# Performance work log

Measured on AMD Instinct MI355X. Metric: run time of the kernel, lower is better.

The kernel has to match this reference:

```python
import jax, jax.numpy as jnp
import numpy as np

COMMITMENT_COST = 1.0


def setup_inputs() -> dict:
    key = jax.random.key(0)
    k1, k2 = jax.random.split(key)
    B, D, H, W = 32, 256, 32, 32
    K = 1024
    z = jax.random.normal(k1, (B, D, H, W), dtype=jnp.float32)
    # torch init: uniform(-1/K, 1/K)
    codebook = jax.random.uniform(k2, (K, D), dtype=jnp.float32,
                                  minval=-1.0 / K, maxval=1.0 / K)
    return {"z": z, "codebook": codebook}


def reference(z, codebook):
    B, D, H, W = z.shape
    # (B, D, H, W) -> (B, H, W, D) -> (N, D)
    zp = jnp.transpose(z, (0, 2, 3, 1))
    zf = zp.reshape(-1, D)
    # squared euclidean distances (N, K): ||z||^2 + ||e||^2 - 2 z.e
    d = (jnp.sum(zf * zf, axis=1, keepdims=True)
         + jnp.sum(codebook * codebook, axis=1)
         - 2.0 * jnp.matmul(zf, codebook.T))
    idx = jnp.argmin(d, axis=1)                    # (N,)
    zq = codebook[idx].reshape(B, H, W, D)         # gather
    vq_loss = jnp.mean((jax.lax.stop_gradient(zq) - zp) ** 2)
    commitment_loss = jnp.mean((zq - jax.lax.stop_gradient(zp)) ** 2)
    loss = vq_loss + COMMITMENT_COST * commitment_loss
    # straight-through estimator
    zq_st = zp + jax.lax.stop_gradient(zq - zp)
    zq_out = jnp.transpose(zq_st, (0, 3, 1, 2))    # back to (B, D, H, W)
    indices = idx.reshape(B, H, W)
    return zq_out, indices, loss
```

## Files before the change

### kernel.cpp

```cpp
#include <hip/hip_runtime.h>

#define NPOS 32768
#define DDIM 256
#define KCODE 1024
#define HW 1024
#define BSTRIDE (256*1024)
#define OUT0_SIZE 8388608
#define OUT1_SIZE 32768

#define WS_ET     0
#define WS_ZN     262144
#define WS_EN     294912
#define WS_PACKED 295936


__global__ void vq_zn(const float* __restrict__ z, float* __restrict__ zn,
                      unsigned long long* __restrict__ packed,
                      float* __restrict__ loss_slot) {
    int n = blockIdx.x * 256 + threadIdx.x;
    int b = n >> 10, hw = n & 1023;
    const float* zp = z + (size_t)b * BSTRIDE + hw;
    float half_s[2];
    #pragma unroll
    for (int h = 0; h < 2; ++h) {
        const float* p = zp + (size_t)(h * 128) * HW;
        float r[8];
        #pragma unroll
        for (int j = 0; j < 8; ++j) {
            float v = p[(size_t)j * HW];
            r[j] = __fmul_rn(v, v);
        }
        #pragma unroll
        for (int i = 8; i < 128; i += 8) {
            #pragma unroll
            for (int j = 0; j < 8; ++j) {
                float v = p[(size_t)(i + j) * HW];
                r[j] = __fadd_rn(r[j], __fmul_rn(v, v));
            }
        }
        half_s[h] = __fadd_rn(
            __fadd_rn(__fadd_rn(r[0], r[1]), __fadd_rn(r[2], r[3])),
            __fadd_rn(__fadd_rn(r[4], r[5]), __fadd_rn(r[6], r[7])));
    }
    zn[n] = __fadd_rn(half_s[0], half_s[1]);
    packed[n] = 0xFFFFFFFFFFFFFFFFull;
    if (n == 0) *loss_slot = 0.0f;
}

__global__ void vq_en(const float* __restrict__ cb, float* __restrict__ en) {
    int k = blockIdx.x * 256 + threadIdx.x;
    const float* row = cb + (size_t)k * DDIM;
    float half_s[2];
    #pragma unroll
    for (int h = 0; h < 2; ++h) {
        const float* p = row + h * 128;
        float r[8];
        #pragma unroll
        for (int j = 0; j < 8; ++j) r[j] = __fmul_rn(p[j], p[j]);
        #pragma unroll
        for (int i = 8; i < 128; i += 8) {
            #pragma unroll
            for (int j = 0; j < 8; ++j)
                r[j] = __fadd_rn(r[j], __fmul_rn(p[i + j], p[i + j]));
        }
        half_s[h] = __fadd_rn(
            __fadd_rn(__fadd_rn(r[0], r[1]), __fadd_rn(r[2], r[3])),
            __fadd_rn(__fadd_rn(r[4], r[5]), __fadd_rn(r[6], r[7])));
    }
    en[k] = __fadd_rn(half_s[0], half_s[1]);
}

__global__ void vq_trans(const float* __restrict__ cb, float* __restrict__ et) {
    __shared__ float tile[64][65];
    int k0 = (blockIdx.x & 15) * 64;
    int d0 = (blockIdx.x >> 4) * 64;
    int t = threadIdx.x;
    #pragma unroll
    for (int p = 0; p < 4; ++p) {
        int r  = p * 16 + (t >> 4);
        int c4 = (t & 15) * 4;
        float4 v = *reinterpret_cast<const float4*>(
            cb + (size_t)(k0 + r) * DDIM + d0 + c4);
        tile[r][c4] = v.x; tile[r][c4+1] = v.y;
        tile[r][c4+2] = v.z; tile[r][c4+3] = v.w;
    }
    __syncthreads();
    #pragma unroll
    for (int s = 0; s < 16; ++s) {
        int dd = s * 4 + (t >> 6);
        int kk = t & 63;
        et[(size_t)(d0 + dd) * KCODE + k0 + kk] = tile[kk][dd];
    }
}

#define BM 64
#define BN 256
#define BK 16
#define BSKEW(k) ((k) + ((k) >> 3))

__launch_bounds__(256, 4)
__global__ void vq_argmin(const float* __restrict__ z,
                          const float* __restrict__ ws_f,
                          unsigned long long* __restrict__ packed) {
    __shared__ float As[BK][64];
    __shared__ float Bs[BK][288];

    const float* ET  = ws_f + WS_ET;
    const float* znW = ws_f + WS_ZN;
    const float* enW = ws_f + WS_EN;

    int t  = threadIdx.x;
    int tx = t & 31;
    int ty = t >> 5;
    int bc = blockIdx.x & 3;
    int bm = blockIdx.x >> 2;
    int kc = bc * BN;
    int n0 = bm * BM;
    int b  = n0 >> 10, hw0 = n0 & 1023;
    const float* zb = z + (size_t)b * BSTRIDE + hw0;

    float znr[8];
    #pragma unroll
    for (int j = 0; j < 8; ++j) znr[j] = znW[n0 + ty * 8 + j];

    float acc[8][8];
    #pragma unroll
    for (int j = 0; j < 8; ++j)
        #pragma unroll
        for (int c = 0; c < 8; ++c) acc[j][c] = 0.0f;

    for (int d0 = 0; d0 < DDIM; d0 += BK) {
        __syncthreads();
        {
            int dk = t >> 4, p4 = (t & 15) << 2;
            float4 v = *reinterpret_cast<const float4*>(
                zb + (size_t)(d0 + dk) * HW + p4);
            As[dk][p4] = v.x; As[dk][p4+1] = v.y;
            As[dk][p4+2] = v.z; As[dk][p4+3] = v.w;
        }
        #pragma unroll
        for (int i = 0; i < 4; ++i) {
            int q = t + i * 256;
            int dk = q >> 6, m = q & 63;
            float4 v = *reinterpret_cast<const float4*>(
                ET + (size_t)(d0 + dk) * KCODE + kc + 4 * m);
            int ph = BSKEW(4 * m);
            *reinterpret_cast<float4*>(&Bs[dk][ph]) = v;
        }
        __syncthreads();

        #pragma unroll
        for (int dk = 0; dk < BK; ++dk) {
            float4 a0 = *reinterpret_cast<const float4*>(&As[dk][ty * 8]);
            float4 a1 = *reinterpret_cast<const float4*>(&As[dk][ty * 8 + 4]);
            float4 b0 = *reinterpret_cast<const float4*>(&Bs[dk][9 * tx]);
            float4 b1 = *reinterpret_cast<const float4*>(&Bs[dk][9 * tx + 4]);
            float a[8]  = {a0.x, a0.y, a0.z, a0.w, a1.x, a1.y, a1.z, a1.w};
            float bb[8] = {b0.x, b0.y, b0.z, b0.w, b1.x, b1.y, b1.z, b1.w};
            #pragma unroll
            for (int j = 0; j < 8; ++j)
                #pragma unroll
                for (int c = 0; c < 8; ++c)
                    acc[j][c] = fmaf(a[j], bb[c], acc[j][c]);
        }
    }

    float m1[8];
    int   i1[8];
    #pragma unroll
    for (int j = 0; j < 8; ++j) { m1[j] = 1e30f; i1[j] = 0; }
    #pragma unroll
    for (int c = 0; c < 8; ++c) {
        int k = kc + tx * 8 + c;
        float ek = enW[k];
        #pragma unroll
        for (int j = 0; j < 8; ++j) {
            float t1 = __fadd_rn(znr[j], ek);
            float d  = __fsub_rn(t1, __fmul_rn(2.0f, acc[j][c]));
            if (d < m1[j]) { m1[j] = d; i1[j] = k; }
        }
    }

    #pragma unroll
    for (int j = 0; j < 8; ++j) {
        float a1 = m1[j];
        int   ii = i1[j];
        #pragma unroll
        for (int off = 1; off < 32; off <<= 1) {
            float o1 = __shfl_xor(a1, off, 32);
            int   oi = __shfl_xor(ii, off, 32);
            if (o1 < a1 || (o1 == a1 && oi < ii)) { a1 = o1; ii = oi; }
        }
        if (tx == 0) {
            unsigned long long key =
                ((unsigned long long)__float_as_uint(a1) << 32) |
                (unsigned long long)(unsigned)ii;
            atomicMin(&packed[n0 + ty * 8 + j], key);
        }
    }
}

__global__ void vq_gather(const float* __restrict__ z,
                          const float* __restrict__ cb,
                          const unsigned long long* __restrict__ packed,
                          float* __restrict__ out,
                          float* __restrict__ loss) {
    int n = blockIdx.x * 256 + threadIdx.x;
    int b = n >> 10, hw = n & 1023;
    int k = (int)(unsigned)(packed[n] & 0xFFFFFFFFull);
    const float* e  = cb + (size_t)k * DDIM;
    const float* zp = z + (size_t)b * BSTRIDE + hw;
    float* op = out + (size_t)b * BSTRIDE + hw;
    float s = 0.0f;
    #pragma unroll 4
    for (int d = 0; d < DDIM; ++d) {
        float ev = e[d];
        float zv = zp[(size_t)d * HW];
        op[(size_t)d * HW] = ev;
        float df = ev - zv;
        s = fmaf(df, df, s);
    }
    out[OUT0_SIZE + n] = (float)k;

    #pragma unroll
    for (int off = 32; off > 0; off >>= 1) s += __shfl_down(s, off);
    __shared__ float red[4];
    int lane = threadIdx.x & 63, w = threadIdx.x >> 6;
    if (lane == 0) red[w] = s;
    __syncthreads();
    if (threadIdx.x == 0) {
        float tot = (red[0] + red[1] + red[2] + red[3]) * (2.0f / 8388608.0f);
        atomicAdd(loss, tot);
    }
}

extern "C" void kernel_launch(void* const* d_in, const int* in_sizes, int n_in,
                              void* d_out, int out_size, void* d_ws, size_t ws_size,
                              hipStream_t stream) {
    const float* z  = (const float*)d_in[0];
    const float* cb = (const float*)d_in[1];
    float* out  = (float*)d_out;
    float* ws_f = (float*)d_ws;
    unsigned long long* packed =
        (unsigned long long*)(ws_f + WS_PACKED);
    float* loss = out + OUT0_SIZE + OUT1_SIZE;

    vq_zn<<<NPOS / 256, 256, 0, stream>>>(z, ws_f + WS_ZN, packed, loss);
    vq_en<<<KCODE / 256, 256, 0, stream>>>(cb, ws_f + WS_EN);
    vq_trans<<<64, 256, 0, stream>>>(cb, ws_f + WS_ET);
    vq_argmin<<<(NPOS / BM) * (KCODE / BN), 256, 0, stream>>>(z, ws_f, packed);
    vq_gather<<<NPOS / 256, 256, 0, stream>>>(z, cb, packed, out, loss);
}
```

Measured before the change: 353.4 us.

## Merge prep kernels, read z tile directly from global, vectorize codebook gather

Fuses the zn, en and codebook-transpose kernels into one launch, with separate block ranges doing each job, to save launch overhead. In the argmin GEMM the z tile is no longer staged through shared memory: each thread loads its 8 positions straight from global (cache-backed) memory on every dk step. The gather kernel reads codebook rows as float4 instead of scalars. Skipping the LDS staging removes a store and sync step but raises repeated global/L1 traffic in the inner loop, since the 32 threads sharing a ty load the same addresses.

```diff
diff --git a/kernel.cpp b/kernel.cpp
--- a/kernel.cpp
+++ b/kernel.cpp
@@ -13,83 +13,86 @@
 #define WS_EN     294912
 #define WS_PACKED 295936
 
-
-__global__ void vq_zn(const float* __restrict__ z, float* __restrict__ zn,
-                      unsigned long long* __restrict__ packed,
-                      float* __restrict__ loss_slot) {
-    int n = blockIdx.x * 256 + threadIdx.x;
-    int b = n >> 10, hw = n & 1023;
-    const float* zp = z + (size_t)b * BSTRIDE + hw;
-    float half_s[2];
-    #pragma unroll
-    for (int h = 0; h < 2; ++h) {
-        const float* p = zp + (size_t)(h * 128) * HW;
-        float r[8];
-        #pragma unroll
-        for (int j = 0; j < 8; ++j) {
-            float v = p[(size_t)j * HW];
-            r[j] = __fmul_rn(v, v);
-        }
-        #pragma unroll
-        for (int i = 8; i < 128; i += 8) {
+__global__ void vq_prep(const float* __restrict__ z,
+                        const float* __restrict__ cb,
+                        float* __restrict__ ws_f,
+                        unsigned long long* __restrict__ packed,
+                        float* __restrict__ loss_slot) {
+    __shared__ float tile[64][65];
+    int bx = blockIdx.x;
+    int t  = threadIdx.x;
+
+    if (bx < 128) {
+        int n = bx * 256 + t;
+        int b = n >> 10, hw = n & 1023;
+        const float* zp = z + (size_t)b * BSTRIDE + hw;
+        float half_s[2];
+        #pragma unroll
+        for (int h = 0; h < 2; ++h) {
+            const float* p = zp + (size_t)(h * 128) * HW;
+            float r[8];
             #pragma unroll
             for (int j = 0; j < 8; ++j) {
-                float v = p[(size_t)(i + j) * HW];
-                r[j] = __fadd_rn(r[j], __fmul_rn(v, v));
+                float v = p[(size_t)j * HW];
+                r[j] = __fmul_rn(v, v);
             }
-        }
-        half_s[h] = __fadd_rn(
-            __fadd_rn(__fadd_rn(r[0], r[1]), __fadd_rn(r[2], r[3])),
-            __fadd_rn(__fadd_rn(r[4], r[5]), __fadd_rn(r[6], r[7])));
-    }
-    zn[n] = __fadd_rn(half_s[0], half_s[1]);
-    packed[n] = 0xFFFFFFFFFFFFFFFFull;
-    if (n == 0) *loss_slot = 0.0f;
-}
-
-__global__ void vq_en(const float* __restrict__ cb, float* __restrict__ en) {
-    int k = blockIdx.x * 256 + threadIdx.x;
-    const float* row = cb + (size_t)k * DDIM;
-    float half_s[2];
-    #pragma unroll
-    for (int h = 0; h < 2; ++h) {
-        const float* p = row + h * 128;
-        float r[8];
-        #pragma unroll
-        for (int j = 0; j < 8; ++j) r[j] = __fmul_rn(p[j], p[j]);
-        #pragma unroll
-        for (int i = 8; i < 128; i += 8) {
-            #pragma unroll
-            for (int j = 0; j < 8; ++j)
-                r[j] = __fadd_rn(r[j], __fmul_rn(p[i + j], p[i + j]));
-        }
-        half_s[h] = __fadd_rn(
-            __fadd_rn(__fadd_rn(r[0], r[1]), __fadd_rn(r[2], r[3])),
-            __fadd_rn(__fadd_rn(r[4], r[5]), __fadd_rn(r[6], r[7])));
-    }
-    en[k] = __fadd_rn(half_s[0], half_s[1]);
-}
-
-__global__ void vq_trans(const float* __restrict__ cb, float* __restrict__ et) {
-    __shared__ float tile[64][65];
-    int k0 = (blockIdx.x & 15) * 64;
-    int d0 = (blockIdx.x >> 4) * 64;
-    int t = threadIdx.x;
-    #pragma unroll
-    for (int p = 0; p < 4; ++p) {
-        int r  = p * 16 + (t >> 4);
-        int c4 = (t & 15) * 4;
-        float4 v = *reinterpret_cast<const float4*>(
-            cb + (size_t)(k0 + r) * DDIM + d0 + c4);
-        tile[r][c4] = v.x; tile[r][c4+1] = v.y;
-        tile[r][c4+2] = v.z; tile[r][c4+3] = v.w;
-    }
-    __syncthreads();
-    #pragma unroll
-    for (int s = 0; s < 16; ++s) {
-        int dd = s * 4 + (t >> 6);
-        int kk = t & 63;
-        et[(size_t)(d0 + dd) * KCODE + k0 + kk] = tile[kk][dd];
+            #pragma unroll
+            for (int i = 8; i < 128; i += 8) {
+                #pragma unroll
+                for (int j = 0; j < 8; ++j) {
+                    float v = p[(size_t)(i + j) * HW];
+                    r[j] = __fadd_rn(r[j], __fmul_rn(v, v));
+                }
+            }
+            half_s[h] = __fadd_rn(
+                __fadd_rn(__fadd_rn(r[0], r[1]), __fadd_rn(r[2], r[3])),
+                __fadd_rn(__fadd_rn(r[4], r[5]), __fadd_rn(r[6], r[7])));
+        }
+        ws_f[WS_ZN + n] = __fadd_rn(half_s[0], half_s[1]);
+        packed[n] = 0xFFFFFFFFFFFFFFFFull;
+        if (n == 0) *loss_slot = 0.0f;
+    } else if (bx < 132) {
+        int k = (bx - 128) * 256 + t;
+        const float* row = cb + (size_t)k * DDIM;
+        float half_s[2];
+        #pragma unroll
+        for (int h = 0; h < 2; ++h) {
+            const float* p = row + h * 128;
+            float r[8];
+            #pragma unroll
+            for (int j = 0; j < 8; ++j) r[j] = __fmul_rn(p[j], p[j]);
+            #pragma unroll
+            for (int i = 8; i < 128; i += 8) {
+                #pragma unroll
+                for (int j = 0; j < 8; ++j)
+                    r[j] = __fadd_rn(r[j], __fmul_rn(p[i + j], p[i + j]));
+            }
+            half_s[h] = __fadd_rn(
+                __fadd_rn(__fadd_rn(r[0], r[1]), __fadd_rn(r[2], r[3])),
+                __fadd_rn(__fadd_rn(r[4], r[5]), __fadd_rn(r[6], r[7])));
+        }
+        ws_f[WS_EN + k] = __fadd_rn(half_s[0], half_s[1]);
+    } else {
+        int bt = bx - 132;
+        int k0 = (bt & 15) * 64;
+        int d0 = (bt >> 4) * 64;
+        float* et = ws_f + WS_ET;
+        #pragma unroll
+        for (int p = 0; p < 4; ++p) {
+            int r  = p * 16 + (t >> 4);
+            int c4 = (t & 15) * 4;
+            float4 v = *reinterpret_cast<const float4*>(
+                cb + (size_t)(k0 + r) * DDIM + d0 + c4);
+            tile[r][c4] = v.x; tile[r][c4+1] = v.y;
+            tile[r][c4+2] = v.z; tile[r][c4+3] = v.w;
+        }
+        __syncthreads();
+        #pragma unroll
+        for (int s = 0; s < 16; ++s) {
+            int dd = s * 4 + (t >> 6);
+            int kk = t & 63;
+            et[(size_t)(d0 + dd) * KCODE + k0 + kk] = tile[kk][dd];
+        }
     }
 }
 
@@ -102,7 +105,6 @@
 __global__ void vq_argmin(const float* __restrict__ z,
                           const float* __restrict__ ws_f,
                           unsigned long long* __restrict__ packed) {
-    __shared__ float As[BK][64];
     __shared__ float Bs[BK][288];
 
     const float* ET  = ws_f + WS_ET;
@@ -118,6 +120,7 @@
     int n0 = bm * BM;
     int b  = n0 >> 10, hw0 = n0 & 1023;
     const float* zb = z + (size_t)b * BSTRIDE + hw0;
+    const float* za = zb + ty * 8;
 
     float znr[8];
     #pragma unroll
@@ -131,13 +134,6 @@
 
     for (int d0 = 0; d0 < DDIM; d0 += BK) {
         __syncthreads();
-        {
-            int dk = t >> 4, p4 = (t & 15) << 2;
-            float4 v = *reinterpret_cast<const float4*>(
-                zb + (size_t)(d0 + dk) * HW + p4);
-            As[dk][p4] = v.x; As[dk][p4+1] = v.y;
-            As[dk][p4+2] = v.z; As[dk][p4+3] = v.w;
-        }
         #pragma unroll
         for (int i = 0; i < 4; ++i) {
             int q = t + i * 256;
@@ -151,8 +147,10 @@
 
         #pragma unroll
         for (int dk = 0; dk < BK; ++dk) {
-            float4 a0 = *reinterpret_cast<const float4*>(&As[dk][ty * 8]);
-            float4 a1 = *reinterpret_cast<const float4*>(&As[dk][ty * 8 + 4]);
+            float4 a0 = *reinterpret_cast<const float4*>(
+                za + (size_t)(d0 + dk) * HW);
+            float4 a1 = *reinterpret_cast<const float4*>(
+                za + (size_t)(d0 + dk) * HW + 4);
             float4 b0 = *reinterpret_cast<const float4*>(&Bs[dk][9 * tx]);
             float4 b1 = *reinterpret_cast<const float4*>(&Bs[dk][9 * tx + 4]);
             float a[8]  = {a0.x, a0.y, a0.z, a0.w, a1.x, a1.y, a1.z, a1.w};
@@ -213,12 +211,17 @@
     float* op = out + (size_t)b * BSTRIDE + hw;
     float s = 0.0f;
     #pragma unroll 4
-    for (int d = 0; d < DDIM; ++d) {
-        float ev = e[d];
-        float zv = zp[(size_t)d * HW];
-        op[(size_t)d * HW] = ev;
-        float df = ev - zv;
-        s = fmaf(df, df, s);
+    for (int d4 = 0; d4 < DDIM / 4; ++d4) {
+        float4 ev = *reinterpret_cast<const float4*>(e + 4 * d4);
+        float evs[4] = {ev.x, ev.y, ev.z, ev.w};
+        #pragma unroll
+        for (int q = 0; q < 4; ++q) {
+            int d = 4 * d4 + q;
+            float zv = zp[(size_t)d * HW];
+            op[(size_t)d * HW] = evs[q];
+            float df = evs[q] - zv;
+            s = fmaf(df, df, s);
+        }
     }
     out[OUT0_SIZE + n] = (float)k;
 
@@ -245,9 +248,7 @@
         (unsigned long long*)(ws_f + WS_PACKED);
     float* loss = out + OUT0_SIZE + OUT1_SIZE;
 
-    vq_zn<<<NPOS / 256, 256, 0, stream>>>(z, ws_f + WS_ZN, packed, loss);
-    vq_en<<<KCODE / 256, 256, 0, stream>>>(cb, ws_f + WS_EN);
-    vq_trans<<<64, 256, 0, stream>>>(cb, ws_f + WS_ET);
+    vq_prep<<<196, 256, 0, stream>>>(z, cb, ws_f, packed, loss);
     vq_argmin<<<(NPOS / BM) * (KCODE / BN), 256, 0, stream>>>(z, ws_f, packed);
     vq_gather<<<NPOS / 256, 256, 0, stream>>>(z, cb, packed, out, loss);
 }
```

Measured after the change: 512.9 us. 45.1% more time.
